# Optimization experiments

Measured on AMD Instinct MI355X. Metric: run time of the kernel, lower is better.

Reference implementation:

```python
import jax, jax.numpy as jnp
import numpy as np
from jax import lax

GROUPS = 4
KH = KW = 3
K = KH * KW
STRIDE = (1, 1)
PAD = ((1, 1), (1, 1))
DIL = (1, 1)


def _bilinear_gather(padded, py, px):
    # padded: (B,C,Hp,Wp); py,px: (B,C,K,Ho,Wo) float sample positions in padded coords
    B, C, Hp, Wp = padded.shape
    bi = jnp.arange(B)[:, None, None, None, None]
    ci = jnp.arange(C)[None, :, None, None, None]
    y0 = jnp.floor(py)
    x0 = jnp.floor(px)
    wy = py - y0
    wx = px - x0
    out = jnp.zeros(py.shape, padded.dtype)
    corners = ((0, 0, (1 - wy) * (1 - wx)), (0, 1, (1 - wy) * wx),
               (1, 0, wy * (1 - wx)), (1, 1, wy * wx))
    for dy, dx, w in corners:
        yy = y0 + dy
        xx = x0 + dx
        valid = (yy >= 0) & (yy < Hp) & (xx >= 0) & (xx < Wp)  # zero outside (implicit zero padding)
        yc = jnp.clip(yy, 0, Hp - 1).astype(jnp.int32)
        xc = jnp.clip(xx, 0, Wp - 1).astype(jnp.int32)
        out = out + jnp.where(valid, padded[bi, ci, yc, xc] * w, 0.0)
    return out


def deform_conv2d(inps, weight, bias, weight_off, bias_off):
    B, C, H, W = inps.shape
    # offset/mask predicting conv (grouped, same geometry as the main conv)
    off = lax.conv_general_dilated(inps, weight_off, STRIDE, PAD, rhs_dilation=DIL,
                                   feature_group_count=GROUPS,
                                   dimension_numbers=('NCHW', 'OIHW', 'NCHW'))
    off = off + bias_off[None, :, None, None]
    Ho, Wo = off.shape[2], off.shape[3]
    off = off.reshape(B, 3, C * K, Ho, Wo)  # (B, dim+1, C*K, Ho, Wo)
    dy = off[:, 0].reshape(B, C, K, Ho, Wo)
    dx = off[:, 1].reshape(B, C, K, Ho, Wo)
    # softmax across the GROUP axis, as in the original reshape(b,1,groups,-1,h,w).softmax(dim=2)
    mask = jax.nn.softmax(off[:, 2].reshape(B, GROUPS, (C // GROUPS) * K, Ho, Wo), axis=1)
    mask = mask.reshape(B, C, K, Ho, Wo)

    padded = jnp.pad(inps, ((0, 0), (0, 0), PAD[0], PAD[1]))
    ky, kx = jnp.meshgrid(jnp.arange(KH), jnp.arange(KW), indexing='ij')
    ky = ky.ravel().astype(inps.dtype)
    kx = kx.ravel().astype(inps.dtype)
    oh = jnp.arange(Ho, dtype=inps.dtype)
    ow = jnp.arange(Wo, dtype=inps.dtype)
    # sample position per (batch, in-channel, kernel tap, output pixel)
    py = oh[None, None, None, :, None] * STRIDE[0] + ky[None, None, :, None, None] * DIL[0] + dy
    px = ow[None, None, None, None, :] * STRIDE[1] + kx[None, None, :, None, None] * DIL[1] + dx

    sampled = _bilinear_gather(padded, py, px) * mask  # (B,C,K,Ho,Wo)

    Cout = weight.shape[0]
    Cg = C // GROUPS
    wg = weight.reshape(GROUPS, Cout // GROUPS, Cg, K)          # (g, o, c, k)
    sg = sampled.reshape(B, GROUPS, Cg, K, Ho, Wo)              # (b, g, c, k, h, w)
    out = jnp.einsum('bgckhw,gock->bgohw', sg, wg).reshape(B, Cout, Ho, Wo)
    return out + bias[None, :, None, None]


def setup_inputs() -> dict:
    key = jax.random.key(0)
    k0, k1, k2, k3 = jax.random.split(key, 4)
    B, C, H, W = 8, 64, 64, 64
    Cout = 64
    inps = jax.random.normal(k0, (B, C, H, W), dtype=jnp.float32)
    weight = jax.random.normal(k1, (Cout, C // GROUPS, KH, KW), dtype=jnp.float32) * 0.05
    bias = jax.random.normal(k2, (Cout,), dtype=jnp.float32) * 0.05
    # small offset-conv weights -> offsets of a few pixels, non-saturated softmax
    weight_off = jax.random.normal(k3, (C * K * 3, C // GROUPS, KH, KW), dtype=jnp.float32) * 0.05
    bias_off = jnp.zeros((C * K * 3,), dtype=jnp.float32)
    return {'inps': inps, 'weight': weight, 'bias': bias,
            'weight_off': weight_off, 'bias_off': bias_off}


def reference(inps, weight, bias, weight_off, bias_off):
    return deform_conv2d(inps, weight, bias, weight_off, bias_off)
```

## Files before the change

### kernel.cpp

```cpp
#include <hip/hip_runtime.h>

typedef __attribute__((ext_vector_type(8))) short short8;
typedef __attribute__((ext_vector_type(4))) float f32x4;

__device__ __forceinline__ unsigned short bf16rne(float f) {
    unsigned u = __float_as_uint(f);
    u += 0x7FFFu + ((u >> 16) & 1u);
    return (unsigned short)(u >> 16);
}
__device__ __forceinline__ float bf16dec(unsigned short h) {
    return __uint_as_float((unsigned)h << 16);
}
__device__ __forceinline__ unsigned cvtpk2(float lo, float hi) {
    unsigned r;
    asm("v_cvt_pk_bf16_f32 %0, %1, %2" : "=v"(r) : "v"(lo), "v"(hi));
    return r;
}

extern __shared__ char smem[];


#define IMC6_OFF   0
#define PATCH6_OFF 37376
#define SX6_OFF    62720
#define LGX6_OFF   72960
#define LDS_V6     81664
#define OTB6_OFF   37376

#define PWOFF_U32  138240
#define PWM_U32    5120
#define WS_NEEDED  ((size_t)(PWOFF_U32 + PWM_U32) * 4)

__global__ __launch_bounds__(256)
void pack_weights(const float* __restrict__ wmain,
                  const float* __restrict__ woff,
                  unsigned* __restrict__ pw)
{
    int idx = blockIdx.x * 256 + threadIdx.x;
    if (idx < PWOFF_U32) {
        int j2   = idx & 3;
        int lane = (idx >> 2) & 63;
        int rest = idx >> 8;
        int kt   = rest % 5;
        int t    = rest / 5;
        int comp = t / 36, r36 = t - comp * 36;
        int jw   = r36 / 9, ntg = r36 - jw * 9;
        int ochb = comp * 576 + jw * 144 + ntg * 16;
        int g    = ochb / 432;
        int ktf  = (9 * g) >> 1;
        int och  = ochb + (lane & 15);
        int ck   = (ktf + kt) * 32 + (lane >> 4) * 8 + j2 * 2 - g * 144;
        float v0 = 0.f, v1 = 0.f;
        if ((unsigned)ck < 144u)       v0 = woff[(size_t)och * 144 + ck];
        if ((unsigned)(ck + 1) < 144u) v1 = woff[(size_t)och * 144 + ck + 1];
        pw[idx] = (unsigned)bf16rne(v0) | ((unsigned)bf16rne(v1) << 16);
    } else if (idx < PWOFF_U32 + PWM_U32) {
        int m    = idx - PWOFF_U32;
        int j2   = m & 3;
        int lane = (m >> 2) & 63;
        int rest = m >> 8;
        int jw   = rest / 5, pair = rest - jw * 5;
        int och  = jw * 16 + (lane & 15);
        int w0   = pair * 32 + (lane >> 4) * 8 + j2 * 2;
        float v0 = (w0 < 144)     ? wmain[(size_t)och * 144 + w0]     : 0.f;
        float v1 = (w0 + 1 < 144) ? wmain[(size_t)och * 144 + w0 + 1] : 0.f;
        pw[idx] = (unsigned)bf16rne(v0) | ((unsigned)bf16rne(v1) << 16);
    }
}

__global__ __launch_bounds__(256, 2)
void deform_v6(const float* __restrict__ inps,
               const float* __restrict__ bmain,
               const float* __restrict__ boff,
               const unsigned short* __restrict__ pwoff,
               const unsigned short* __restrict__ pwm,
               float* __restrict__ out)
{
    unsigned short* IMC   = (unsigned short*)(smem + IMC6_OFF);
    unsigned short* PATCH = (unsigned short*)(smem + PATCH6_OFF);
    unsigned short* SX    = (unsigned short*)(smem + SX6_OFF);
    unsigned short* LGX   = (unsigned short*)(smem + LGX6_OFF);
    float*          OTB   = (float*)(smem + OTB6_OFF);

    const int tid  = threadIdx.x;
    const int lane = tid & 63;
    const int jw   = __builtin_amdgcn_readfirstlane(tid >> 6);
    const int slot = lane & 15;
    const int q    = lane >> 4;

    const int b    = blockIdx.x >> 7;
    const int tile = blockIdx.x & 127;
    const int ty0  = (tile >> 3) << 2;
    const int tx0  = (tile & 7) << 3;

    const float* inb = inps + (size_t)b * 262144;

    for (int e = tid; e < 12288; e += 256) {
        int c = e / 192, rem = e - c * 192;
        int y = rem >> 4, x = rem & 15;
        int gy = ty0 + y - 4, gx = tx0 + x - 4;
        float v = 0.f;
        if ((unsigned)gy < 64u && (unsigned)gx < 64u)
            v = inb[(c * 64 + gy) * 64 + gx];
        PATCH[c * 198 + rem] = bf16rne(v);
    }
    __syncthreads();

    {
        const int px  = tid >> 3;
        const int sub = tid & 7;
        const int pyr = px >> 3, pxx = px & 7;
        unsigned* dst = (unsigned*)(IMC + px * 584);
        #pragma unroll 4
        for (int i = 0; i < 36; ++i) {
            int kk = i * 16 + sub * 2;
            int c0 = kk / 9,        r0 = kk - c0 * 9;
            int c1 = (kk + 1) / 9,  r1 = (kk + 1) - c1 * 9;
            unsigned short a  = PATCH[c0 * 198 + (pyr + r0 / 3 + 3) * 16 + pxx + r0 % 3 + 3];
            unsigned short bb = PATCH[c1 * 198 + (pyr + r1 / 3 + 3) * 16 + pxx + r1 % 3 + 3];
            dst[(unsigned)kk >> 1] = (unsigned)a | ((unsigned)bb << 16);
        }
    }
    __syncthreads();

    f32x4 aco[2] = {{0.f,0.f,0.f,0.f},{0.f,0.f,0.f,0.f}};

    auto pair_mfma = [&](int pair) {
        const short8 bfr = ((const short8*)pwm)[(jw * 5 + pair) * 64 + lane];
        #pragma unroll
        for (int mt = 0; mt < 2; ++mt) {
            const short8 a8 = *(const short8*)(SX + jw * 1280 + (mt * 16 + slot) * 40 + q * 8);
            aco[mt] = __builtin_amdgcn_mfma_f32_16x16x32_bf16(a8, bfr, aco[mt], 0, 0, 0);
        }
    };

    for (int ntg = 0; ntg < 9; ++ntg) {
        const int lb = (ntg & 1) * 2176;

        f32x4 aD[2] = {{0.f,0.f,0.f,0.f},{0.f,0.f,0.f,0.f}};
        f32x4 aX[2] = {{0.f,0.f,0.f,0.f},{0.f,0.f,0.f,0.f}};
        f32x4 aM[2] = {{0.f,0.f,0.f,0.f},{0.f,0.f,0.f,0.f}};

        auto gemm3 = [&](f32x4* acc, int comp) {
            const int ochb = comp * 576 + jw * 144 + ntg * 16;
            const int g    = ochb / 432;
            const int ktf  = (9 * g) >> 1;
            const int t    = comp * 36 + jw * 9 + ntg;
            const short8* wp  = (const short8*)pwoff + t * 320 + lane;
            const short8* ap0 = (const short8*)(smem + IMC6_OFF);
            short8 bw[5];
            #pragma unroll
            for (int kt = 0; kt < 5; ++kt) bw[kt] = wp[kt * 64];
            #pragma unroll
            for (int kt = 0; kt < 5; ++kt) {
                const int ktg = ktf + kt;
                #pragma unroll
                for (int mt = 0; mt < 2; ++mt) {
                    const short8 af = ap0[(mt * 16 + slot) * 73 + ktg * 4 + q];
                    acc[mt] = __builtin_amdgcn_mfma_f32_16x16x32_bf16(af, bw[kt], acc[mt], 0, 0, 0);
                }
            }
            const float bo = boff[ochb + slot];
            #pragma unroll
            for (int mt = 0; mt < 2; ++mt) {
                acc[mt][0] += bo; acc[mt][1] += bo; acc[mt][2] += bo; acc[mt][3] += bo;
            }
        };
        gemm3(aD, 0); gemm3(aX, 1); gemm3(aM, 2);

        #pragma unroll
        for (int mt = 0; mt < 2; ++mt)
        #pragma unroll
        for (int r = 0; r < 4; ++r) {
            int pxr = mt * 16 + q * 4 + r;
            LGX[lb + pxr * 68 + slot * 4 + jw] = bf16rne(aM[mt][r]);
        }
        __syncthreads();

        const int rr  = ntg * 16 + slot;
        const int cg  = rr / 9;
        const int kk9 = rr - cg * 9;
        const int kyk = kk9 / 3, kxk = kk9 - kyk * 3;
        const int c   = jw * 16 + cg;
        const float* inc = inb + c * 4096;
        const int pbase = c * 198;
        const int par = ntg & 1;

        #pragma unroll
        for (int mt = 0; mt < 2; ++mt)
        #pragma unroll
        for (int r = 0; r < 4; ++r) {
            const int pxr = mt * 16 + q * 4 + r;
            const int pyr = pxr >> 3, pxx = pxr & 7;
            const float own = aM[mt][r];

            const uint2 lg = *(const uint2*)(LGX + lb + pxr * 68 + slot * 4);
            float s4 = __expf(bf16dec((unsigned short)(lg.x & 0xFFFF)) - own)
                     + __expf(bf16dec((unsigned short)(lg.x >> 16))    - own)
                     + __expf(bf16dec((unsigned short)(lg.y & 0xFFFF)) - own)
                     + __expf(bf16dec((unsigned short)(lg.y >> 16))    - own);
            const float msk = 1.0f / s4;

            float pyf = (float)(ty0 + pyr + kyk - 1) + aD[mt][r];
            float pxf = (float)(tx0 + pxx + kxk - 1) + aX[mt][r];
            float y0f = floorf(pyf), x0f = floorf(pxf);
            float wy = pyf - y0f, wx = pxf - x0f;
            int iy0 = (int)y0f, ix0 = (int)x0f;

            int ly0 = iy0 - ty0 + 4;
            int lx0 = ix0 - tx0 + 4;
            float v;
            if ((unsigned)ly0 < 11u && (unsigned)lx0 < 15u) {
                const int a = pbase + ly0 * 16 + lx0;
                float p00 = bf16dec(PATCH[a]),      p01 = bf16dec(PATCH[a + 1]);
                float p10 = bf16dec(PATCH[a + 16]), p11 = bf16dec(PATCH[a + 17]);
                float top = fmaf(wx, p01 - p00, p00);
                float bot = fmaf(wx, p11 - p10, p10);
                v = fmaf(wy, bot - top, top);
            } else {
                float w00 = (1.f - wy) * (1.f - wx), w01 = (1.f - wy) * wx;
                float w10 = wy * (1.f - wx),         w11 = wy * wx;
                v = 0.f;
                if ((unsigned)iy0 < 64u) {
                    if ((unsigned)ix0 < 64u)       v += w00 * inc[iy0 * 64 + ix0];
                    if ((unsigned)(ix0 + 1) < 64u) v += w01 * inc[iy0 * 64 + ix0 + 1];
                }
                if ((unsigned)(iy0 + 1) < 64u) {
                    if ((unsigned)ix0 < 64u)       v += w10 * inc[(iy0 + 1) * 64 + ix0];
                    if ((unsigned)(ix0 + 1) < 64u) v += w11 * inc[(iy0 + 1) * 64 + ix0 + 1];
                }
            }
            SX[jw * 1280 + pxr * 40 + par * 16 + slot] = bf16rne(v * msk);
        }

        if (ntg & 1)  { asm volatile("" ::: "memory"); pair_mfma(ntg >> 1); }
        if (ntg == 8) { asm volatile("" ::: "memory"); pair_mfma(4); }
    }
    __syncthreads();

    {
        const int o = jw * 16 + slot;
        const float bo = bmain[o];
        #pragma unroll
        for (int mt = 0; mt < 2; ++mt)
        #pragma unroll
        for (int r = 0; r < 4; ++r)
            OTB[o * 33 + mt * 16 + q * 4 + r] = aco[mt][r] + bo;
    }
    __syncthreads();
    #pragma unroll
    for (int i = 0; i < 8; ++i) {
        int f  = i * 256 + tid;
        int oo = f >> 5, pp = f & 31;
        out[(size_t)(b * 64 + oo) * 4096 + (ty0 + (pp >> 3)) * 64 + (tx0 + (pp & 7))] =
            OTB[oo * 33 + pp];
    }
}

#define V2IMC_OFF   0
#define V2S_OFF     37376
#define V2LGX_OFF   74752
#define V2LDS_BYTES 78848

__global__ __launch_bounds__(256, 2)
void deform_v2(const float* __restrict__ inps,
               const float* __restrict__ wmain,
               const float* __restrict__ bmain,
               const float* __restrict__ woff,
               const float* __restrict__ boff,
               float* __restrict__ out)
{
    unsigned short* IMC  = (unsigned short*)(smem + V2IMC_OFF);
    unsigned short* SBUF = (unsigned short*)(smem + V2S_OFF);
    unsigned short* LGX  = (unsigned short*)(smem + V2LGX_OFF);
    float* PATCH = (float*)(smem + V2S_OFF);
    float* OTB   = (float*)(smem + V2IMC_OFF);

    const int tid  = threadIdx.x;
    const int lane = tid & 63;
    const int jw   = __builtin_amdgcn_readfirstlane(tid >> 6);
    const int slot = lane & 15;
    const int q    = lane >> 4;

    const int b    = blockIdx.x >> 7;
    const int tile = blockIdx.x & 127;
    const int ty0  = (tile >> 3) << 2;
    const int tx0  = (tile & 7) << 3;

    const float* inb = inps + (size_t)b * 262144;

    for (int e = tid; e < 64 * 60; e += 256) {
        int ch = e / 60, rem = e - ch * 60;
        int iy = rem / 10, ix = rem - iy * 10;
        int gy = ty0 + iy - 1, gx = tx0 + ix - 1;
        float v = 0.f;
        if ((unsigned)gy < 64u && (unsigned)gx < 64u)
            v = inb[(ch * 64 + gy) * 64 + gx];
        PATCH[ch * 61 + rem] = v;
    }
    __syncthreads();
    {
        const int px  = tid >> 3;
        const int sub = tid & 7;
        const int pyr = px >> 3, pxx = px & 7;
        unsigned short* dst = IMC + px * 584;
        for (int i = 0; i < 36; ++i) {
            int kk = sub * 72 + 2 * i;
            float v0, v1;
            { int c = kk / 9, r9 = kk - c * 9, ky = r9 / 3, kx = r9 - ky * 3;
              v0 = PATCH[c * 61 + (pyr + ky) * 10 + (pxx + kx)]; }
            { int k1 = kk + 1; int c = k1 / 9, r9 = k1 - c * 9, ky = r9 / 3, kx = r9 - ky * 3;
              v1 = PATCH[c * 61 + (pyr + ky) * 10 + (pxx + kx)]; }
            *(unsigned*)(dst + kk) = cvtpk2(v0, v1);
        }
    }
    __syncthreads();

    for (int ntg = 0; ntg < 9; ++ntg) {
        f32x4 aD[2] = {{0.f,0.f,0.f,0.f},{0.f,0.f,0.f,0.f}};
        f32x4 aX[2] = {{0.f,0.f,0.f,0.f},{0.f,0.f,0.f,0.f}};
        f32x4 aM[2] = {{0.f,0.f,0.f,0.f},{0.f,0.f,0.f,0.f}};

        auto gemm3 = [&](f32x4* acc, int comp) {
            const int ochb = comp * 576 + jw * 144 + ntg * 16;
            const int g    = ochb / 432;
            const int ktf  = (9 * g) >> 1;
            const int ch0  = g * 18;
            const int och  = ochb + slot;
            #pragma unroll
            for (int kt = 0; kt < 5; ++kt) {
                const int ktg   = ktf + kt;
                const int chunk = ktg * 4 + q;
                short8 bfr;
                if ((unsigned)(chunk - ch0) < 18u) {
                    const float4* wp = (const float4*)(woff + (size_t)och * 144 + (chunk - ch0) * 8);
                    float4 w0 = wp[0], w1 = wp[1];
                    union { unsigned u[4]; short8 s; } cv;
                    cv.u[0] = cvtpk2(w0.x, w0.y); cv.u[1] = cvtpk2(w0.z, w0.w);
                    cv.u[2] = cvtpk2(w1.x, w1.y); cv.u[3] = cvtpk2(w1.z, w1.w);
                    bfr = cv.s;
                } else {
                    bfr = short8{0,0,0,0,0,0,0,0};
                }
                #pragma unroll
                for (int mt = 0; mt < 2; ++mt) {
                    const short8* ap = (const short8*)(smem + V2IMC_OFF +
                                        (mt * 16 + slot) * 1168 + ktg * 64 + q * 16);
                    acc[mt] = __builtin_amdgcn_mfma_f32_16x16x32_bf16(*ap, bfr, acc[mt], 0, 0, 0);
                }
            }
            const float bo = boff[ochb + slot];
            #pragma unroll
            for (int mt = 0; mt < 2; ++mt) {
                acc[mt][0] += bo; acc[mt][1] += bo; acc[mt][2] += bo; acc[mt][3] += bo;
            }
        };
        gemm3(aD, 0); gemm3(aX, 1); gemm3(aM, 2);

        #pragma unroll
        for (int mt = 0; mt < 2; ++mt)
        #pragma unroll
        for (int r = 0; r < 4; ++r) {
            int pxr = mt * 16 + q * 4 + r;
            LGX[(jw * 32 + pxr) * 16 + slot] = bf16rne(aM[mt][r]);
        }
        __syncthreads();

        const int rr  = ntg * 16 + slot;
        const int cg  = rr / 9;
        const int kk9 = rr - cg * 9;
        const int kyk = kk9 / 3, kxk = kk9 - kyk * 3;
        const float* inc = inb + (jw * 16 + cg) * 4096;

        #pragma unroll
        for (int mt = 0; mt < 2; ++mt)
        #pragma unroll
        for (int r = 0; r < 4; ++r) {
            const int pxr = mt * 16 + q * 4 + r;
            const int pyr = pxr >> 3, pxx = pxr & 7;
            float own = aM[mt][r];
            float l0 = (jw == 0) ? own : bf16dec(LGX[(0 * 32 + pxr) * 16 + slot]);
            float l1 = (jw == 1) ? own : bf16dec(LGX[(1 * 32 + pxr) * 16 + slot]);
            float l2 = (jw == 2) ? own : bf16dec(LGX[(2 * 32 + pxr) * 16 + slot]);
            float l3 = (jw == 3) ? own : bf16dec(LGX[(3 * 32 + pxr) * 16 + slot]);
            float m4 = fmaxf(fmaxf(l0, l1), fmaxf(l2, l3));
            float s4 = __expf(l0 - m4) + __expf(l1 - m4) + __expf(l2 - m4) + __expf(l3 - m4);
            float msk = __expf(own - m4) / s4;

            float pyf = (float)(ty0 + pyr + kyk - 1) + aD[mt][r];
            float pxf = (float)(tx0 + pxx + kxk - 1) + aX[mt][r];
            float y0f = floorf(pyf), x0f = floorf(pxf);
            float wy = pyf - y0f, wx = pxf - x0f;
            int iy0 = (int)y0f, ix0 = (int)x0f;
            float w00 = (1.f - wy) * (1.f - wx), w01 = (1.f - wy) * wx;
            float w10 = wy * (1.f - wx),         w11 = wy * wx;
            float v = 0.f;
            if ((unsigned)iy0 < 64u) {
                if ((unsigned)ix0 < 64u)       v += w00 * inc[iy0 * 64 + ix0];
                if ((unsigned)(ix0 + 1) < 64u) v += w01 * inc[iy0 * 64 + ix0 + 1];
            }
            if ((unsigned)(iy0 + 1) < 64u) {
                if ((unsigned)ix0 < 64u)       v += w10 * inc[(iy0 + 1) * 64 + ix0];
                if ((unsigned)(ix0 + 1) < 64u) v += w11 * inc[(iy0 + 1) * 64 + ix0 + 1];
            }
            SBUF[pxr * 584 + jw * 144 + rr] = bf16rne(v * msk);
        }
        __syncthreads();
    }

    {
        f32x4 aco2[2] = {{0.f,0.f,0.f,0.f},{0.f,0.f,0.f,0.f}};
        const int ktf = (9 * jw) >> 1;
        const int ch0 = jw * 18;
        const int o   = jw * 16 + slot;
        #pragma unroll
        for (int kt = 0; kt < 5; ++kt) {
            const int ktg   = ktf + kt;
            const int chunk = ktg * 4 + q;
            short8 bfr;
            if ((unsigned)(chunk - ch0) < 18u) {
                const float4* wp = (const float4*)(wmain + (size_t)o * 144 + (chunk - ch0) * 8);
                float4 w0 = wp[0], w1 = wp[1];
                union { unsigned u[4]; short8 s; } cv;
                cv.u[0] = cvtpk2(w0.x, w0.y); cv.u[1] = cvtpk2(w0.z, w0.w);
                cv.u[2] = cvtpk2(w1.x, w1.y); cv.u[3] = cvtpk2(w1.z, w1.w);
                bfr = cv.s;
            } else {
                bfr = short8{0,0,0,0,0,0,0,0};
            }
            #pragma unroll
            for (int mt = 0; mt < 2; ++mt) {
                const short8* ap = (const short8*)(smem + V2S_OFF +
                                    (mt * 16 + slot) * 1168 + ktg * 64 + q * 16);
                aco2[mt] = __builtin_amdgcn_mfma_f32_16x16x32_bf16(*ap, bfr, aco2[mt], 0, 0, 0);
            }
        }
        const float bo = bmain[o];
        __syncthreads();
        #pragma unroll
        for (int mt = 0; mt < 2; ++mt)
        #pragma unroll
        for (int r = 0; r < 4; ++r)
            OTB[o * 33 + mt * 16 + q * 4 + r] = aco2[mt][r] + bo;
    }
    __syncthreads();
    #pragma unroll
    for (int i = 0; i < 8; ++i) {
        int f  = i * 256 + tid;
        int oo = f >> 5, pp = f & 31;
        out[(size_t)(b * 64 + oo) * 4096 + (ty0 + (pp >> 3)) * 64 + (tx0 + (pp & 7))] =
            OTB[oo * 33 + pp];
    }
}

extern "C" void kernel_launch(void* const* d_in, const int* in_sizes, int n_in,
                              void* d_out, int out_size, void* d_ws, size_t ws_size,
                              hipStream_t stream) {
    const float* inps   = (const float*)d_in[0];
    const float* weight = (const float*)d_in[1];
    const float* bias   = (const float*)d_in[2];
    const float* woff   = (const float*)d_in[3];
    const float* boff   = (const float*)d_in[4];
    float* outp = (float*)d_out;

    if (ws_size >= WS_NEEDED) {
        unsigned* pw = (unsigned*)d_ws;
        pack_weights<<<dim3(560), dim3(256), 0, stream>>>(weight, woff, pw);
        hipFuncSetAttribute((const void*)deform_v6,
                            hipFuncAttributeMaxDynamicSharedMemorySize, LDS_V6);
        deform_v6<<<dim3(1024), dim3(256), LDS_V6, stream>>>(
            inps, bias, boff,
            (const unsigned short*)pw,
            (const unsigned short*)(pw + PWOFF_U32), outp);
    } else {
        hipFuncSetAttribute((const void*)deform_v2,
                            hipFuncAttributeMaxDynamicSharedMemorySize, V2LDS_BYTES);
        deform_v2<<<dim3(1024), dim3(256), V2LDS_BYTES, stream>>>(
            inps, weight, bias, woff, boff, outp);
    }
}
```

Baseline: 136.6 us.

## Split pixel-row tiles across eight waves and use exp2 for softmax

Doubles the block to 512 threads, giving each of eight waves one 16-pixel M-tile instead of two, so per-wave MFMA chains, accumulators and sampling work are halved. Loaders and the output store are rescaled to match. Mask logits are pre-scaled by log2(e) so the softmax can use exp2f instead of __expf. The extra waves raise parallelism and latency hiding per block, but the per-pixel weight fragment loads are now repeated by two waves, and LDS use is unchanged, so fewer waves may fit per CU.

```diff
diff --git a/kernel.cpp b/kernel.cpp
--- a/kernel.cpp
+++ b/kernel.cpp
@@ -20,12 +20,14 @@
 extern __shared__ char smem[];
 
 
-#define IMC6_OFF   0
-#define PATCH6_OFF 37376
-#define SX6_OFF    62720
-#define LGX6_OFF   72960
-#define LDS_V6     81664
-#define OTB6_OFF   37376
+#define IMC7_OFF   0
+#define PATCH7_OFF 37376
+#define SX7_OFF    62720
+#define LGX7_OFF   72960
+#define LDS_V7     81664
+#define OTB7_OFF   37376
+
+#define LOG2E 1.4426950408889634f
 
 #define PWOFF_U32  138240
 #define PWM_U32    5120
@@ -68,23 +70,25 @@
     }
 }
 
-__global__ __launch_bounds__(256, 2)
-void deform_v6(const float* __restrict__ inps,
+__global__ __launch_bounds__(512, 2)
+void deform_v7(const float* __restrict__ inps,
                const float* __restrict__ bmain,
                const float* __restrict__ boff,
                const unsigned short* __restrict__ pwoff,
                const unsigned short* __restrict__ pwm,
                float* __restrict__ out)
 {
-    unsigned short* IMC   = (unsigned short*)(smem + IMC6_OFF);
-    unsigned short* PATCH = (unsigned short*)(smem + PATCH6_OFF);
-    unsigned short* SX    = (unsigned short*)(smem + SX6_OFF);
-    unsigned short* LGX   = (unsigned short*)(smem + LGX6_OFF);
-    float*          OTB   = (float*)(smem + OTB6_OFF);
+    unsigned short* IMC   = (unsigned short*)(smem + IMC7_OFF);
+    unsigned short* PATCH = (unsigned short*)(smem + PATCH7_OFF);
+    unsigned short* SX    = (unsigned short*)(smem + SX7_OFF);
+    unsigned short* LGX   = (unsigned short*)(smem + LGX7_OFF);
+    float*          OTB   = (float*)(smem + OTB7_OFF);
 
     const int tid  = threadIdx.x;
     const int lane = tid & 63;
-    const int jw   = __builtin_amdgcn_readfirstlane(tid >> 6);
+    const int wv   = __builtin_amdgcn_readfirstlane(tid >> 6);
+    const int jw   = wv & 3;
+    const int mtw  = wv >> 2;
     const int slot = lane & 15;
     const int q    = lane >> 4;
 
@@ -95,7 +99,7 @@
 
     const float* inb = inps + (size_t)b * 262144;
 
-    for (int e = tid; e < 12288; e += 256) {
+    for (int e = tid; e < 12288; e += 512) {
         int c = e / 192, rem = e - c * 192;
         int y = rem >> 4, x = rem & 15;
         int gy = ty0 + y - 4, gx = tx0 + x - 4;
@@ -107,73 +111,64 @@
     __syncthreads();
 
     {
-        const int px  = tid >> 3;
-        const int sub = tid & 7;
+        const int px  = tid >> 4;
+        const int sub = tid & 15;
         const int pyr = px >> 3, pxx = px & 7;
         unsigned* dst = (unsigned*)(IMC + px * 584);
-        #pragma unroll 4
-        for (int i = 0; i < 36; ++i) {
-            int kk = i * 16 + sub * 2;
+        #pragma unroll 3
+        for (int i = 0; i < 18; ++i) {
+            int u  = i * 16 + sub;
+            int kk = u * 2;
             int c0 = kk / 9,        r0 = kk - c0 * 9;
             int c1 = (kk + 1) / 9,  r1 = (kk + 1) - c1 * 9;
             unsigned short a  = PATCH[c0 * 198 + (pyr + r0 / 3 + 3) * 16 + pxx + r0 % 3 + 3];
             unsigned short bb = PATCH[c1 * 198 + (pyr + r1 / 3 + 3) * 16 + pxx + r1 % 3 + 3];
-            dst[(unsigned)kk >> 1] = (unsigned)a | ((unsigned)bb << 16);
-        }
-    }
-    __syncthreads();
-
-    f32x4 aco[2] = {{0.f,0.f,0.f,0.f},{0.f,0.f,0.f,0.f}};
+            dst[u] = (unsigned)a | ((unsigned)bb << 16);
+        }
+    }
+    __syncthreads();
+
+    f32x4 aco = {0.f, 0.f, 0.f, 0.f};
 
     auto pair_mfma = [&](int pair) {
         const short8 bfr = ((const short8*)pwm)[(jw * 5 + pair) * 64 + lane];
-        #pragma unroll
-        for (int mt = 0; mt < 2; ++mt) {
-            const short8 a8 = *(const short8*)(SX + jw * 1280 + (mt * 16 + slot) * 40 + q * 8);
-            aco[mt] = __builtin_amdgcn_mfma_f32_16x16x32_bf16(a8, bfr, aco[mt], 0, 0, 0);
-        }
+        const short8 a8  = *(const short8*)(SX + jw * 1280 + (mtw * 16 + slot) * 40 + q * 8);
+        aco = __builtin_amdgcn_mfma_f32_16x16x32_bf16(a8, bfr, aco, 0, 0, 0);
     };
 
     for (int ntg = 0; ntg < 9; ++ntg) {
         const int lb = (ntg & 1) * 2176;
 
-        f32x4 aD[2] = {{0.f,0.f,0.f,0.f},{0.f,0.f,0.f,0.f}};
-        f32x4 aX[2] = {{0.f,0.f,0.f,0.f},{0.f,0.f,0.f,0.f}};
-        f32x4 aM[2] = {{0.f,0.f,0.f,0.f},{0.f,0.f,0.f,0.f}};
-
-        auto gemm3 = [&](f32x4* acc, int comp) {
+        f32x4 aD = {0.f,0.f,0.f,0.f};
+        f32x4 aX = {0.f,0.f,0.f,0.f};
+        f32x4 aM = {0.f,0.f,0.f,0.f};
+
+        auto gemm3 = [&](f32x4& acc, int comp) {
             const int ochb = comp * 576 + jw * 144 + ntg * 16;
             const int g    = ochb / 432;
             const int ktf  = (9 * g) >> 1;
             const int t    = comp * 36 + jw * 9 + ntg;
             const short8* wp  = (const short8*)pwoff + t * 320 + lane;
-            const short8* ap0 = (const short8*)(smem + IMC6_OFF);
+            const short8* ap0 = (const short8*)(smem + IMC7_OFF);
             short8 bw[5];
             #pragma unroll
             for (int kt = 0; kt < 5; ++kt) bw[kt] = wp[kt * 64];
             #pragma unroll
             for (int kt = 0; kt < 5; ++kt) {
-                const int ktg = ktf + kt;
-                #pragma unroll
-                for (int mt = 0; mt < 2; ++mt) {
-                    const short8 af = ap0[(mt * 16 + slot) * 73 + ktg * 4 + q];
-                    acc[mt] = __builtin_amdgcn_mfma_f32_16x16x32_bf16(af, bw[kt], acc[mt], 0, 0, 0);
-                }
+                const short8 af = ap0[(mtw * 16 + slot) * 73 + (ktf + kt) * 4 + q];
+                acc = __builtin_amdgcn_mfma_f32_16x16x32_bf16(af, bw[kt], acc, 0, 0, 0);
             }
             const float bo = boff[ochb + slot];
-            #pragma unroll
-            for (int mt = 0; mt < 2; ++mt) {
-                acc[mt][0] += bo; acc[mt][1] += bo; acc[mt][2] += bo; acc[mt][3] += bo;
-            }
+            acc[0] += bo; acc[1] += bo; acc[2] += bo; acc[3] += bo;
         };
         gemm3(aD, 0); gemm3(aX, 1); gemm3(aM, 2);
 
-        #pragma unroll
-        for (int mt = 0; mt < 2; ++mt)
+        aM[0] *= LOG2E; aM[1] *= LOG2E; aM[2] *= LOG2E; aM[3] *= LOG2E;
+
         #pragma unroll
         for (int r = 0; r < 4; ++r) {
-            int pxr = mt * 16 + q * 4 + r;
-            LGX[lb + pxr * 68 + slot * 4 + jw] = bf16rne(aM[mt][r]);
+            int pxr = mtw * 16 + q * 4 + r;
+            LGX[lb + pxr * 68 + slot * 4 + jw] = bf16rne(aM[r]);
         }
         __syncthreads();
 
@@ -187,22 +182,20 @@
         const int par = ntg & 1;
 
         #pragma unroll
-        for (int mt = 0; mt < 2; ++mt)
-        #pragma unroll
         for (int r = 0; r < 4; ++r) {
-            const int pxr = mt * 16 + q * 4 + r;
+            const int pxr = mtw * 16 + q * 4 + r;
             const int pyr = pxr >> 3, pxx = pxr & 7;
-            const float own = aM[mt][r];
+            const float own = aM[r];
 
             const uint2 lg = *(const uint2*)(LGX + lb + pxr * 68 + slot * 4);
-            float s4 = __expf(bf16dec((unsigned short)(lg.x & 0xFFFF)) - own)
-                     + __expf(bf16dec((unsigned short)(lg.x >> 16))    - own)
-                     + __expf(bf16dec((unsigned short)(lg.y & 0xFFFF)) - own)
-                     + __expf(bf16dec((unsigned short)(lg.y >> 16))    - own);
+            float s4 = exp2f(bf16dec((unsigned short)(lg.x & 0xFFFF)) - own)
+                     + exp2f(bf16dec((unsigned short)(lg.x >> 16))    - own)
+                     + exp2f(bf16dec((unsigned short)(lg.y & 0xFFFF)) - own)
+                     + exp2f(bf16dec((unsigned short)(lg.y >> 16))    - own);
             const float msk = 1.0f / s4;
 
-            float pyf = (float)(ty0 + pyr + kyk - 1) + aD[mt][r];
-            float pxf = (float)(tx0 + pxx + kxk - 1) + aX[mt][r];
+            float pyf = (float)(ty0 + pyr + kyk - 1) + aD[r];
+            float pxf = (float)(tx0 + pxx + kxk - 1) + aX[r];
             float y0f = floorf(pyf), x0f = floorf(pxf);
             float wy = pyf - y0f, wx = pxf - x0f;
             int iy0 = (int)y0f, ix0 = (int)x0f;
@@ -242,15 +235,13 @@
         const int o = jw * 16 + slot;
         const float bo = bmain[o];
         #pragma unroll
-        for (int mt = 0; mt < 2; ++mt)
-        #pragma unroll
         for (int r = 0; r < 4; ++r)
-            OTB[o * 33 + mt * 16 + q * 4 + r] = aco[mt][r] + bo;
+            OTB[o * 33 + mtw * 16 + q * 4 + r] = aco[r] + bo;
     }
     __syncthreads();
     #pragma unroll
-    for (int i = 0; i < 8; ++i) {
-        int f  = i * 256 + tid;
+    for (int i = 0; i < 4; ++i) {
+        int f  = i * 512 + tid;
         int oo = f >> 5, pp = f & 31;
         out[(size_t)(b * 64 + oo) * 4096 + (ty0 + (pp >> 3)) * 64 + (tx0 + (pp & 7))] =
             OTB[oo * 33 + pp];
@@ -466,9 +457,9 @@
     if (ws_size >= WS_NEEDED) {
         unsigned* pw = (unsigned*)d_ws;
         pack_weights<<<dim3(560), dim3(256), 0, stream>>>(weight, woff, pw);
-        hipFuncSetAttribute((const void*)deform_v6,
-                            hipFuncAttributeMaxDynamicSharedMemorySize, LDS_V6);
-        deform_v6<<<dim3(1024), dim3(256), LDS_V6, stream>>>(
+        hipFuncSetAttribute((const void*)deform_v7,
+                            hipFuncAttributeMaxDynamicSharedMemorySize, LDS_V7);
+        deform_v7<<<dim3(1024), dim3(512), LDS_V7, stream>>>(
             inps, bias, boff,
             (const unsigned short*)pw,
             (const unsigned short*)(pw + PWOFF_U32), outp);
```

After: 124.4 us. 9.0% less time.
